# Optimization experiments

Measured on AMD Instinct MI355X. Metric: run time of the kernel, lower is better.

Reference implementation:

```python
import jax, jax.numpy as jnp
import numpy as np

T, D, H, B = 2048, 1152, 16, 8
DH = D // H  # 72


def _apply_rope(x, cos_h, sin_h):
    # x: [T, H, DH]; cos_h, sin_h: [T, DH//2] (already chunked halves)
    c = jnp.concatenate([cos_h, cos_h], axis=-1)[:, None, :]  # [T,1,DH]
    s = jnp.concatenate([sin_h, sin_h], axis=-1)[:, None, :]
    x1, x2 = jnp.split(x, 2, axis=-1)
    rot = jnp.concatenate([-x2, x1], axis=-1)
    return x * c + rot * s


def setup_inputs() -> dict:
    key = jax.random.key(0)
    ks = jax.random.split(key, 12)
    hidden_states = jax.random.normal(ks[0], (T, D), jnp.float32)
    inner = jnp.sort(jax.random.randint(ks[1], (B - 1,), 1, T))
    cu_seqlens = jnp.concatenate(
        [jnp.zeros((1,), jnp.int32), inner.astype(jnp.int32), jnp.full((1,), T, jnp.int32)])
    cos = jax.random.uniform(ks[2], (T, DH), jnp.float32, -1.0, 1.0)
    sin = jax.random.uniform(ks[3], (T, DH), jnp.float32, -1.0, 1.0)
    std = 0.02
    Wq = jax.random.normal(ks[4], (D, D), jnp.float32) * std
    Wk = jax.random.normal(ks[5], (D, D), jnp.float32) * std
    Wv = jax.random.normal(ks[6], (D, D), jnp.float32) * std
    Wo = jax.random.normal(ks[7], (D, D), jnp.float32) * std
    bq = jnp.zeros((D,), jnp.float32)
    bk = jnp.zeros((D,), jnp.float32)
    bv = jnp.zeros((D,), jnp.float32)
    bo = jnp.zeros((D,), jnp.float32)
    return {"hidden_states": hidden_states, "cu_seqlens": cu_seqlens,
            "cos": cos, "sin": sin,
            "Wq": Wq, "bq": bq, "Wk": Wk, "bk": bk,
            "Wv": Wv, "bv": bv, "Wo": Wo, "bo": bo}


def reference(hidden_states, cu_seqlens, cos, sin, Wq, bq, Wk, bk, Wv, bv, Wo, bo):
    t = hidden_states.shape[0]
    scale = DH ** -0.5
    q = (hidden_states @ Wq.T + bq).reshape(t, H, DH)
    k = (hidden_states @ Wk.T + bk).reshape(t, H, DH)
    v = (hidden_states @ Wv.T + bv).reshape(t, H, DH)
    # RoPE: cos/sin [T, DH] are chunked in half along last dim, first half used
    cos_h = cos[:, : DH // 2]
    sin_h = sin[:, : DH // 2]
    q = _apply_rope(q, cos_h, sin_h)
    k = _apply_rope(k, cos_h, sin_h)
    # segment ids from cu_seqlens -> block-diagonal (varlen) attention mask
    pos = jnp.arange(t)
    seg = jnp.searchsorted(cu_seqlens, pos, side='right') - 1  # [T]
    mask = seg[:, None] == seg[None, :]  # [T, T]
    scores = jnp.einsum('thd,shd->hts', q, k) * scale  # [H, T, T]
    scores = jnp.where(mask[None], scores, jnp.float32(-1e30))
    attn = jax.nn.softmax(scores, axis=-1)
    out = jnp.einsum('hts,shd->thd', attn, v).reshape(t, D)
    return out @ Wo.T + bo
```

## Files before the change

### kernel.cpp

```cpp
#include <hip/hip_runtime.h>

#define TT 2048
#define DM 1152
#define NHEAD 16
#define HDIM 72
#define HDP 96
#define HDV 80
#define KSPLIT 2

typedef __attribute__((ext_vector_type(8))) __bf16 bf16x8;
typedef __attribute__((ext_vector_type(4))) float f32x4;
typedef unsigned short u16;
typedef unsigned int u32;
typedef __attribute__((ext_vector_type(4))) u16 u16x4;

__device__ inline u16 f2bf(float f){
  u32 u = __builtin_bit_cast(u32, f);
  return (u16)((u + 0x7FFFu + ((u >> 16) & 1u)) >> 16);
}
__device__ inline float bf2f(u16 v){
  return __builtin_bit_cast(float, ((u32)v) << 16);
}
__device__ inline bf16x8 ldb8(const u16* p){
  uint4 u = *(const uint4*)p;
  return __builtin_bit_cast(bf16x8, u);
}
__device__ inline f32x4 mfma16(bf16x8 a, bf16x8 b, f32x4 c){
  return __builtin_amdgcn_mfma_f32_16x16x32_bf16(a, b, c, 0, 0, 0);
}
__device__ inline void gload_lds16(const u16* g, u16* l){
  __builtin_amdgcn_global_load_lds(
      (const __attribute__((address_space(1))) void*)g,
      (__attribute__((address_space(3))) void*)l, 16, 0, 0);
}

__global__ void k_convert(const float* hid, const float* wq, const float* wk,
                          const float* wv, const float* wo, const int* cu,
                          u16* hb, u16* wqb, u16* wkb, u16* wvb, u16* wob,
                          u16* qhb, u16* khb, int* seg)
{
  long i = (long)blockIdx.x * blockDim.x + threadIdx.x;
  const long NHID4 = (long)TT * DM / 4;
  const long NW4 = (long)DM * DM / 4;
  const long NC4 = NHID4 + 4*NW4;
  if (i < NC4) {
    const float4* src; u16* dst; long o;
    if (i < NHID4) { src = (const float4*)hid; dst = hb; o = i; }
    else {
      long j = i - NHID4;
      int w = (int)(j / NW4);
      o = j - (long)w * NW4;
      src = (const float4*)((w==0)?wq:(w==1)?wk:(w==2)?wv:wo);
      dst = (w==0)?wqb:(w==1)?wkb:(w==2)?wvb:wob;
    }
    float4 v = src[o];
    u16x4 r; r.x = f2bf(v.x); r.y = f2bf(v.y); r.z = f2bf(v.z); r.w = f2bf(v.w);
    *(u16x4*)(dst + o*4) = r;
  } else {
    long j = i - NC4;
    const long PER = (long)NHEAD*TT*12;
    if (j < 2*PER) {
      int arr = (int)(j / PER);
      long r = j - (long)arr*PER;
      long th = r / 12;
      int c = (int)(r - th*12);
      ((u32*)(arr ? khb : qhb))[th*48 + 36 + c] = 0u;
    }
  }
  if (i < TT) {
    int c = 0;
    for (int e = 0; e < 9; ++e) c += (cu[e] <= (int)i);
    seg[i] = c - 1;
  }
}

__device__ __forceinline__ void gemm_m128n64(const u16* __restrict__ A,
                                             const u16* __restrict__ W,
                                             const float* __restrict__ bias,
                                             void* out, int mode, float oscale)
{
  __shared__ __align__(16) u16 As[2][128*32];
  __shared__ __align__(16) u16 Bs[2][64*32];
  int tid = threadIdx.x;
  int lane = tid & 63, wid = tid >> 6;
  int l15 = lane & 15, quad = lane >> 4;
  int bm = blockIdx.x * 128, bn = blockIdx.y * 64;
  int wm = wid*32;
  f32x4 acc[2][4] = {};
  const u16* ga = A + (long)(bm + (tid>>2))*DM + (tid&3)*8;
  const u16* gb = W + (long)(bn + (tid>>2))*DM + (tid&3)*8;
  {
    u16* lA = As[0] + wid*512; u16* lB = Bs[0] + wid*512;
    gload_lds16(ga,          lA);
    gload_lds16(ga + 64*DM,  lA + 2048);
    gload_lds16(gb,          lB);
  }
  int cur = 0;
  for (int k0 = 0; k0 < DM; k0 += 32, cur ^= 1) {
    __syncthreads();
    if (k0 + 32 < DM) {
      u16* lA = As[cur^1] + wid*512; u16* lB = Bs[cur^1] + wid*512;
      gload_lds16(ga + k0 + 32,          lA);
      gload_lds16(ga + k0 + 32 + 64*DM,  lA + 2048);
      gload_lds16(gb + k0 + 32,          lB);
    }
    bf16x8 af[2], bfr[4];
    for (int i=0;i<2;i++) af[i]  = ldb8(As[cur] + (wm + i*16 + l15)*32 + quad*8);
    for (int i=0;i<4;i++) bfr[i] = ldb8(Bs[cur] + (i*16 + l15)*32 + quad*8);
    for (int mi=0;mi<2;mi++)
      for (int ni=0;ni<4;ni++)
        acc[mi][ni] = mfma16(af[mi], bfr[ni], acc[mi][ni]);
  }
  for (int ni=0;ni<4;ni++){
    int n = bn + ni*16 + l15;
    float bv_ = bias[n];
    int h = n / HDIM, dh = n - (n / HDIM)*HDIM;
    for (int mi=0;mi<2;mi++){
      int m0 = bm + wm + mi*16 + quad*4;
      for (int r=0;r<4;r++){
        float v = (acc[mi][ni][r] + bv_) * oscale;
        int m = m0 + r;
        if (mode == 0) {
          ((u16*)out)[((long)(h*TT + m))*HDP + dh] = f2bf(v);
        } else {
          ((u16*)out)[((long)(h*HDV + dh))*TT + m] = f2bf(v);
        }
      }
    }
  }
}

__global__ __launch_bounds__(256, 4) void k_gemm_qkv(const u16* __restrict__ A,
    const u16* __restrict__ Wq, const u16* __restrict__ Wk, const u16* __restrict__ Wv,
    const float* __restrict__ bq, const float* __restrict__ bk, const float* __restrict__ bv,
    u16* oq, u16* ok, u16* ov)
{
  const float scale = 0.11785113019775793f;
  int z = blockIdx.z;
  if (z == 0)      gemm_m128n64(A, Wq, bq, oq, 0, scale);
  else if (z == 1) gemm_m128n64(A, Wk, bk, ok, 0, 1.0f);
  else             gemm_m128n64(A, Wv, bv, ov, 2, 1.0f);
}

__global__ __launch_bounds__(256, 4) void k_gemm_o(const u16* __restrict__ A,
    const u16* __restrict__ W, const float* __restrict__ bias, float* out)
{
  __shared__ __align__(16) u16 As[2][64*32];
  __shared__ __align__(16) u16 Bs[2][64*32];
  int tid = threadIdx.x;
  int lane = tid & 63, wid = tid >> 6;
  int l15 = lane & 15, quad = lane >> 4;
  int bm = blockIdx.x * 64, bn = blockIdx.y * 64;
  int wm = (wid>>1)*32, wn = (wid&1)*32;
  f32x4 acc[2][2] = {};
  const u16* ga = A + (long)(bm + (tid>>2))*DM + (tid&3)*8;
  const u16* gb = W + (long)(bn + (tid>>2))*DM + (tid&3)*8;
  {
    gload_lds16(ga, As[0] + wid*512);
    gload_lds16(gb, Bs[0] + wid*512);
  }
  int cur = 0;
  for (int k0 = 0; k0 < DM; k0 += 32, cur ^= 1) {
    __syncthreads();
    if (k0 + 32 < DM) {
      gload_lds16(ga + k0 + 32, As[cur^1] + wid*512);
      gload_lds16(gb + k0 + 32, Bs[cur^1] + wid*512);
    }
    bf16x8 af[2], bfr[2];
    for (int i=0;i<2;i++) af[i]  = ldb8(As[cur] + (wm + i*16 + l15)*32 + quad*8);
    for (int i=0;i<2;i++) bfr[i] = ldb8(Bs[cur] + (wn + i*16 + l15)*32 + quad*8);
    for (int mi=0;mi<2;mi++)
      for (int ni=0;ni<2;ni++)
        acc[mi][ni] = mfma16(af[mi], bfr[ni], acc[mi][ni]);
  }
  for (int ni=0;ni<2;ni++){
    int n = bn + wn + ni*16 + l15;
    float bv_ = bias[n];
    for (int mi=0;mi<2;mi++){
      int m0 = bm + wm + mi*16 + quad*4;
      for (int r=0;r<4;r++)
        out[(long)(m0 + r)*DM + n] = acc[mi][ni][r] + bv_;
    }
  }
}

__global__ void k_rope(u16* qh, u16* kh, const float* __restrict__ cosb,
                       const float* __restrict__ sinb)
{
  int i = blockIdx.x * blockDim.x + threadIdx.x;
  const int total = 2 * NHEAD * TT * 36;
  if (i >= total) return;
  int d = i % 36; int rest = i / 36;
  int t = rest % TT; rest /= TT;
  int h = rest % NHEAD; int qk = rest / NHEAD;
  u16* base = (qk ? kh : qh) + ((long)h*TT + t)*HDP;
  float x1 = bf2f(base[d]), x2 = bf2f(base[d+36]);
  float c = cosb[t*HDIM + d], s = sinb[t*HDIM + d];
  base[d]    = f2bf(x1*c - x2*s);
  base[d+36] = f2bf(x2*c + x1*s);
}

__global__ __launch_bounds__(256) void k_attn(const u16* __restrict__ qh,
                                              const u16* __restrict__ kh,
                                              const u16* __restrict__ vT,
                                              const int* __restrict__ seg,
                                              const int* __restrict__ cu,
                                              float* __restrict__ pacc,
                                              float* __restrict__ plsum)
{
  __shared__ __align__(16) u16 Ks[2][64*96];
  __shared__ __align__(16) u16 pbuf[4][16][72];
  int h = blockIdx.y;
  int z = blockIdx.z;
  int tid = threadIdx.x, lane = tid & 63, wid = tid >> 6;
  int l15 = lane & 15, quad = lane >> 4;
  int qb0 = blockIdx.x * 64;
  int qbase = qb0 + wid*16;

  const u16* qp = qh + ((long)h*TT + qbase + l15)*HDP + quad*8;
  bf16x8 qf0 = ldb8(qp), qf1 = ldb8(qp+32), qf2 = ldb8(qp+64);
  int lo[4], hi[4];
  for (int r=0;r<4;r++){
    int sq = seg[qbase + quad*4 + r];
    lo[r] = cu[sq]; hi[r] = cu[sq+1];
  }
  f32x4 acc[5] = {};
  float lsum[4] = {0.f, 0.f, 0.f, 0.f};

  int s_begin = cu[seg[qb0]] & ~63;
  int s_end = cu[seg[qb0 + 63] + 1];
  int nt = (s_end - s_begin + 63) >> 6;
  int nt0 = (nt + 1) >> 1;
  int it_lo = z ? nt0 : 0;
  int it_hi = z ? nt : nt0;

  const u16* kbase = kh + (long)h*TT*HDP;
  const u16* vbase = vT + ((long)h*HDV + l15)*TT + quad*8;

  if (it_lo < it_hi) {
    {
      const u16* gk = kbase + (long)(s_begin + it_lo*64)*HDP + tid*8;
      u16* lK = Ks[0] + wid*512;
      gload_lds16(gk,        lK);
      gload_lds16(gk + 2048, lK + 2048);
      gload_lds16(gk + 4096, lK + 4096);
    }
    for (int it = it_lo; it < it_hi; ++it) {
      int s0 = s_begin + it*64;
      int cur = (it - it_lo) & 1;
      __syncthreads();
      if (it + 1 < it_hi) {
        const u16* gk = kbase + (long)(s0 + 64)*HDP + tid*8;
        u16* lK = Ks[cur^1] + wid*512;
        gload_lds16(gk,        lK);
        gload_lds16(gk + 2048, lK + 2048);
        gload_lds16(gk + 4096, lK + 4096);
      }
      f32x4 sc[4] = {};
      for (int j=0;j<4;j++){
        const u16* kp = Ks[cur] + (j*16 + l15)*96 + quad*8;
        sc[j] = mfma16(qf0, ldb8(kp),    sc[j]);
        sc[j] = mfma16(qf1, ldb8(kp+32), sc[j]);
        sc[j] = mfma16(qf2, ldb8(kp+64), sc[j]);
      }
      float p[4][4];
      for (int j=0;j<4;j++){
        int kidx = s0 + j*16 + l15;
        for (int r=0;r<4;r++){
          bool in = (kidx >= lo[r]) && (kidx < hi[r]);
          p[j][r] = in ? __expf(sc[j][r]) : 0.f;
          lsum[r] += p[j][r];
        }
      }
      for (int j=0;j<4;j++)
        for (int r=0;r<4;r++)
          pbuf[wid][quad*4+r][j*16+l15] = f2bf(p[j][r]);
      bf16x8 pf0 = ldb8(&pbuf[wid][l15][quad*8]);
      bf16x8 pf1 = ldb8(&pbuf[wid][l15][32 + quad*8]);
      const u16* vp = vbase + s0;
      for (int n=0;n<5;n++){
        bf16x8 vf0 = ldb8(vp + (long)n*16*TT);
        bf16x8 vf1 = ldb8(vp + (long)n*16*TT + 32);
        acc[n] = mfma16(pf0, vf0, acc[n]);
        acc[n] = mfma16(pf1, vf1, acc[n]);
      }
    }
  }
  for (int off=1; off<16; off<<=1)
    for (int r=0;r<4;r++)
      lsum[r] += __shfl_xor(lsum[r], off, 64);
  for (int n=0;n<5;n++){
    int dh = n*16 + l15;
    for (int r=0;r<4;r++){
      int t = qbase + quad*4 + r;
      pacc[(((long)z*TT + t)*NHEAD + h)*HDV + dh] = acc[n][r];
    }
  }
  if (l15 == 0){
    for (int r=0;r<4;r++){
      int t = qbase + quad*4 + r;
      plsum[((long)z*TT + t)*NHEAD + h] = lsum[r];
    }
  }
}

__global__ void k_combine(const float* __restrict__ pacc,
                          const float* __restrict__ plsum,
                          u16* __restrict__ ao)
{
  int i = blockIdx.x*blockDim.x + threadIdx.x;
  const int total = TT*NHEAD*HDIM;
  if (i >= total) return;
  int dh = i % HDIM; int rest = i / HDIM;
  int h = rest % NHEAD; int t = rest / NHEAD;
  long i0 = ((long)t*NHEAD + h)*HDV + dh;
  float a = pacc[i0] + pacc[(long)TT*NHEAD*HDV + i0];
  float l = plsum[t*NHEAD + h] + plsum[TT*NHEAD + t*NHEAD + h];
  ao[(long)t*DM + h*HDIM + dh] = f2bf(a / l);
}

extern "C" void kernel_launch(void* const* d_in, const int* in_sizes, int n_in,
                              void* d_out, int out_size, void* d_ws, size_t ws_size,
                              hipStream_t stream)
{
  const float* hid  = (const float*)d_in[0];
  const int*   cu   = (const int*)d_in[1];
  const float* cosb = (const float*)d_in[2];
  const float* sinb = (const float*)d_in[3];
  const float* wq   = (const float*)d_in[4];
  const float* bq   = (const float*)d_in[5];
  const float* wk   = (const float*)d_in[6];
  const float* bk   = (const float*)d_in[7];
  const float* wv   = (const float*)d_in[8];
  const float* bv   = (const float*)d_in[9];
  const float* wo   = (const float*)d_in[10];
  const float* bo   = (const float*)d_in[11];

  char* ws = (char*)d_ws;
  u16* hb  = (u16*)ws; ws += (long)TT*DM*2;
  u16* wqb = (u16*)ws; ws += (long)DM*DM*2;
  u16* wkb = (u16*)ws; ws += (long)DM*DM*2;
  u16* wvb = (u16*)ws; ws += (long)DM*DM*2;
  u16* wob = (u16*)ws; ws += (long)DM*DM*2;
  u16* qhb = (u16*)ws; ws += (long)NHEAD*TT*HDP*2;
  u16* khb = (u16*)ws; ws += (long)NHEAD*TT*HDP*2;
  u16* vTb = (u16*)ws; ws += (long)NHEAD*HDV*TT*2;
  u16* aob = (u16*)ws; ws += (long)TT*DM*2;
  int* seg = (int*)ws; ws += (long)TT*4;
  float* pacc  = (float*)ws; ws += (long)KSPLIT*TT*NHEAD*HDV*4;
  float* plsum = (float*)ws; ws += (long)KSPLIT*TT*NHEAD*4;

  long nconv = ((long)TT*DM + 4L*DM*DM)/4 + 2L*NHEAD*TT*12;
  k_convert<<<dim3((nconv + 255)/256), 256, 0, stream>>>(
      hid, wq, wk, wv, wo, cu, hb, wqb, wkb, wvb, wob, qhb, khb, seg);

  dim3 gqkv(TT/128, DM/64, 3);
  k_gemm_qkv<<<gqkv, 256, 0, stream>>>(hb, wqb, wkb, wvb, bq, bk, bv, qhb, khb, vTb);

  int nrope = 2*NHEAD*TT*36;
  k_rope<<<dim3((nrope + 255)/256), 256, 0, stream>>>(qhb, khb, cosb, sinb);

  dim3 ga(TT/64, NHEAD, KSPLIT);
  k_attn<<<ga, 256, 0, stream>>>(qhb, khb, vTb, seg, cu, pacc, plsum);

  int ncomb = TT*NHEAD*HDIM;
  k_combine<<<dim3((ncomb + 255)/256), 256, 0, stream>>>(pacc, plsum, aob);

  dim3 go(TT/64, DM/64);
  k_gemm_o<<<go, 256, 0, stream>>>(aob, wob, bo, (float*)d_out);
}
```

Baseline: 203.2 us.

## Process two query sub-tiles per wave in attention to reuse K/V fragments

Each attention block now covers 128 queries instead of 64, with every wave handling two 16-row query tiles. Each K fragment read from LDS and each V fragment read from global memory is used by two MFMAs, halving load traffic per unit of compute. The cost is doubled accumulator and score registers, a larger P staging buffer, half as many blocks (less parallelism), and a wider segment span per block, which can add masked-out key tiles.

```diff
diff --git a/kernel.cpp b/kernel.cpp
--- a/kernel.cpp
+++ b/kernel.cpp
@@ -200,35 +200,38 @@
   base[d+36] = f2bf(x2*c + x1*s);
 }
 
-__global__ __launch_bounds__(256) void k_attn(const u16* __restrict__ qh,
-                                              const u16* __restrict__ kh,
-                                              const u16* __restrict__ vT,
-                                              const int* __restrict__ seg,
-                                              const int* __restrict__ cu,
-                                              float* __restrict__ pacc,
-                                              float* __restrict__ plsum)
+__global__ __launch_bounds__(256, 2) void k_attn(const u16* __restrict__ qh,
+                                                 const u16* __restrict__ kh,
+                                                 const u16* __restrict__ vT,
+                                                 const int* __restrict__ seg,
+                                                 const int* __restrict__ cu,
+                                                 float* __restrict__ pacc,
+                                                 float* __restrict__ plsum)
 {
   __shared__ __align__(16) u16 Ks[2][64*96];
-  __shared__ __align__(16) u16 pbuf[4][16][72];
+  __shared__ __align__(16) u16 pbuf[4][16][144];
   int h = blockIdx.y;
   int z = blockIdx.z;
   int tid = threadIdx.x, lane = tid & 63, wid = tid >> 6;
   int l15 = lane & 15, quad = lane >> 4;
-  int qb0 = blockIdx.x * 64;
-  int qbase = qb0 + wid*16;
-
-  const u16* qp = qh + ((long)h*TT + qbase + l15)*HDP + quad*8;
-  bf16x8 qf0 = ldb8(qp), qf1 = ldb8(qp+32), qf2 = ldb8(qp+64);
-  int lo[4], hi[4];
-  for (int r=0;r<4;r++){
-    int sq = seg[qbase + quad*4 + r];
-    lo[r] = cu[sq]; hi[r] = cu[sq+1];
-  }
-  f32x4 acc[5] = {};
-  float lsum[4] = {0.f, 0.f, 0.f, 0.f};
+  int qb0 = blockIdx.x * 128;
+  int qbase = qb0 + wid*32;
+
+  bf16x8 qf[2][3];
+  int lo[2][4], hi[2][4];
+  for (int t=0;t<2;t++){
+    const u16* qp = qh + ((long)h*TT + qbase + t*16 + l15)*HDP + quad*8;
+    qf[t][0] = ldb8(qp); qf[t][1] = ldb8(qp+32); qf[t][2] = ldb8(qp+64);
+    for (int r=0;r<4;r++){
+      int sq = seg[qbase + t*16 + quad*4 + r];
+      lo[t][r] = cu[sq]; hi[t][r] = cu[sq+1];
+    }
+  }
+  f32x4 acc[2][5] = {};
+  float lsum[2][4] = {};
 
   int s_begin = cu[seg[qb0]] & ~63;
-  int s_end = cu[seg[qb0 + 63] + 1];
+  int s_end = cu[seg[qb0 + 127] + 1];
   int nt = (s_end - s_begin + 63) >> 6;
   int nt0 = (nt + 1) >> 1;
   int it_lo = z ? nt0 : 0;
@@ -256,50 +259,61 @@
         gload_lds16(gk + 2048, lK + 2048);
         gload_lds16(gk + 4096, lK + 4096);
       }
-      f32x4 sc[4] = {};
+      f32x4 sc[2][4] = {};
       for (int j=0;j<4;j++){
         const u16* kp = Ks[cur] + (j*16 + l15)*96 + quad*8;
-        sc[j] = mfma16(qf0, ldb8(kp),    sc[j]);
-        sc[j] = mfma16(qf1, ldb8(kp+32), sc[j]);
-        sc[j] = mfma16(qf2, ldb8(kp+64), sc[j]);
-      }
-      float p[4][4];
-      for (int j=0;j<4;j++){
-        int kidx = s0 + j*16 + l15;
-        for (int r=0;r<4;r++){
-          bool in = (kidx >= lo[r]) && (kidx < hi[r]);
-          p[j][r] = in ? __expf(sc[j][r]) : 0.f;
-          lsum[r] += p[j][r];
+        bf16x8 k0 = ldb8(kp), k1 = ldb8(kp+32), k2 = ldb8(kp+64);
+        sc[0][j] = mfma16(qf[0][0], k0, sc[0][j]);
+        sc[1][j] = mfma16(qf[1][0], k0, sc[1][j]);
+        sc[0][j] = mfma16(qf[0][1], k1, sc[0][j]);
+        sc[1][j] = mfma16(qf[1][1], k1, sc[1][j]);
+        sc[0][j] = mfma16(qf[0][2], k2, sc[0][j]);
+        sc[1][j] = mfma16(qf[1][2], k2, sc[1][j]);
+      }
+      for (int t=0;t<2;t++){
+        for (int j=0;j<4;j++){
+          int kidx = s0 + j*16 + l15;
+          for (int r=0;r<4;r++){
+            bool in = (kidx >= lo[t][r]) && (kidx < hi[t][r]);
+            float p = in ? __expf(sc[t][j][r]) : 0.f;
+            lsum[t][r] += p;
+            pbuf[wid][quad*4+r][t*72 + j*16 + l15] = f2bf(p);
+          }
         }
       }
-      for (int j=0;j<4;j++)
-        for (int r=0;r<4;r++)
-          pbuf[wid][quad*4+r][j*16+l15] = f2bf(p[j][r]);
-      bf16x8 pf0 = ldb8(&pbuf[wid][l15][quad*8]);
-      bf16x8 pf1 = ldb8(&pbuf[wid][l15][32 + quad*8]);
+      bf16x8 pf[2][2];
+      for (int t=0;t<2;t++){
+        pf[t][0] = ldb8(&pbuf[wid][l15][t*72 + quad*8]);
+        pf[t][1] = ldb8(&pbuf[wid][l15][t*72 + 32 + quad*8]);
+      }
       const u16* vp = vbase + s0;
       for (int n=0;n<5;n++){
         bf16x8 vf0 = ldb8(vp + (long)n*16*TT);
         bf16x8 vf1 = ldb8(vp + (long)n*16*TT + 32);
-        acc[n] = mfma16(pf0, vf0, acc[n]);
-        acc[n] = mfma16(pf1, vf1, acc[n]);
+        acc[0][n] = mfma16(pf[0][0], vf0, acc[0][n]);
+        acc[1][n] = mfma16(pf[1][0], vf0, acc[1][n]);
+        acc[0][n] = mfma16(pf[0][1], vf1, acc[0][n]);
+        acc[1][n] = mfma16(pf[1][1], vf1, acc[1][n]);
       }
     }
   }
   for (int off=1; off<16; off<<=1)
-    for (int r=0;r<4;r++)
-      lsum[r] += __shfl_xor(lsum[r], off, 64);
-  for (int n=0;n<5;n++){
-    int dh = n*16 + l15;
-    for (int r=0;r<4;r++){
-      int t = qbase + quad*4 + r;
-      pacc[(((long)z*TT + t)*NHEAD + h)*HDV + dh] = acc[n][r];
-    }
-  }
-  if (l15 == 0){
-    for (int r=0;r<4;r++){
-      int t = qbase + quad*4 + r;
-      plsum[((long)z*TT + t)*NHEAD + h] = lsum[r];
+    for (int t=0;t<2;t++)
+      for (int r=0;r<4;r++)
+        lsum[t][r] += __shfl_xor(lsum[t][r], off, 64);
+  for (int t=0;t<2;t++){
+    for (int n=0;n<5;n++){
+      int dh = n*16 + l15;
+      for (int r=0;r<4;r++){
+        int tk = qbase + t*16 + quad*4 + r;
+        pacc[(((long)z*TT + tk)*NHEAD + h)*HDV + dh] = acc[t][n][r];
+      }
+    }
+    if (l15 == 0){
+      for (int r=0;r<4;r++){
+        int tk = qbase + t*16 + quad*4 + r;
+        plsum[((long)z*TT + tk)*NHEAD + h] = lsum[t][r];
+      }
     }
   }
 }
@@ -360,7 +374,7 @@
   int nrope = 2*NHEAD*TT*36;
   k_rope<<<dim3((nrope + 255)/256), 256, 0, stream>>>(qhb, khb, cosb, sinb);
 
-  dim3 ga(TT/64, NHEAD, KSPLIT);
+  dim3 ga(TT/128, NHEAD, KSPLIT);
   k_attn<<<ga, 256, 0, stream>>>(qhb, khb, vTb, seg, cu, pacc, plsum);
 
   int ncomb = TT*NHEAD*HDIM;
```

New measurement: 198.7 us. -2.2%, faster.
